# Kernel optimization log

Measured on AMD Instinct MI355X. Metric: run time of the kernel, lower is better.

## Reference

```python
import jax, jax.numpy as jnp
import numpy as np
import math

D_MODEL = 256
N_HEADS = 4
D_HEAD = D_MODEL // N_HEADS  # 64
TT_RANK = 4
BATCH = 4
SEQ = 2048


def _xavier(key, shape):
    fan_in, fan_out = shape[0], shape[-1]
    if len(shape) == 4:  # (H, d, d, r) treated roughly like dense xavier
        fan_in, fan_out = shape[1], shape[2] * shape[3]
    lim = math.sqrt(6.0 / (fan_in + fan_out))
    return jax.random.uniform(key, shape, jnp.float32, -lim, lim)


def setup_inputs() -> dict:
    key = jax.random.key(0)
    ks = jax.random.split(key, 12)
    inp = {
        "query": jax.random.normal(ks[0], (BATCH, SEQ, D_MODEL), jnp.float32),
        "key": jax.random.normal(ks[1], (BATCH, SEQ, D_MODEL), jnp.float32),
        "value": jax.random.normal(ks[2], (BATCH, SEQ, D_MODEL), jnp.float32),
        "Wq": _xavier(ks[3], (D_MODEL, D_MODEL)),
        "bq": jnp.zeros((D_MODEL,), jnp.float32),
        "Wk": _xavier(ks[4], (D_MODEL, D_MODEL)),
        "bk": jnp.zeros((D_MODEL,), jnp.float32),
        "Wv": _xavier(ks[5], (D_MODEL, D_MODEL)),
        "bv": jnp.zeros((D_MODEL,), jnp.float32),
        "W2": _xavier(ks[6], (N_HEADS, D_HEAD, D_HEAD, TT_RANK)),
        "alpha": jnp.float32(0.5),  # nonzero so interaction path is exercised
        "Wo": _xavier(ks[7], (D_MODEL, D_MODEL)),
        "bo": jnp.zeros((D_MODEL,), jnp.float32),
    }
    return inp


def reference(query, key, value, Wq, bq, Wk, bk, Wv, bv, W2, alpha, Wo, bo):
    B, Sq, _ = query.shape
    Sk = key.shape[1]
    H, Dh = N_HEADS, D_HEAD

    # projections -> (B, H, S, Dh)
    Q = (query @ Wq + bq).reshape(B, Sq, H, Dh).transpose(0, 2, 1, 3)
    K = (key @ Wk + bk).reshape(B, Sk, H, Dh).transpose(0, 2, 1, 3)
    V = (value @ Wv + bv).reshape(B, Sk, H, Dh).transpose(0, 2, 1, 3)

    scale = math.sqrt(Dh)
    scores = jnp.einsum('bhqd,bhkd->bhqk', Q, K) / scale  # (B,H,Sq,Sk)

    # rank-2 tensor interaction: Qp[b,h,q,a,r] = sum_d Q[b,h,q,d] W2[h,d,a,r]
    #                            Kp[b,h,k,a,r] = sum_e K[b,h,k,e] W2[h,a,e,r]
    Qp = jnp.einsum('bhqd,hdar->bhqar', Q, W2)
    Kp = jnp.einsum('bhke,haer->bhkar', K, W2)
    interaction = jnp.einsum('bhqar,bhkar->bhqk', Qp, Kp) / (Dh * scale)

    total_scores = scores + alpha * interaction
    attn = jax.nn.softmax(total_scores, axis=-1)

    out = jnp.einsum('bhqk,bhkd->bhqd', attn, V)
    out = out.transpose(0, 2, 1, 3).reshape(B, Sq, H * Dh)
    return out @ Wo + bo
```

## Files before the change

kernel.cpp:

```cpp
#include <hip/hip_runtime.h>
#include <hip/hip_bf16.h>

#define BB   4
#define SS   2048
#define DM   256
#define HH   4
#define DHH  64
#define KSPL 4
#define KLEN (SS / KSPL)

typedef unsigned short ushort_t;
typedef unsigned int   uint_t;
using short8   = __attribute__((ext_vector_type(8))) short;
using ushort8  = __attribute__((ext_vector_type(8))) unsigned short;
using ushort4v = __attribute__((ext_vector_type(4))) unsigned short;
using float4v  = __attribute__((ext_vector_type(4))) float;

__device__ __forceinline__ ushort_t f2bf(float f) {
  uint_t u = __float_as_uint(f);
  uint_t r = (u + 0x7FFFu + ((u >> 16) & 1u)) >> 16;
  return (ushort_t)r;
}

__global__ __launch_bounds__(256) void k_pre(
    const float* __restrict__ Wk, const float* __restrict__ Wv,
    const float* __restrict__ Wo, const float* __restrict__ Wq,
    const float* __restrict__ bq, const float* __restrict__ W2,
    const float* __restrict__ alpha_p,
    ushort_t* __restrict__ WkT, ushort_t* __restrict__ WvT,
    ushort_t* __restrict__ WoT, ushort_t* __restrict__ WcT,
    float* __restrict__ bc) {
  __shared__ float sT[64 * 65];
  __shared__ __align__(16) float sM[64];
  const int t = threadIdx.x;
  const int bi = blockIdx.x;
  if (bi < 48) {
    int m = bi >> 4, tile = bi & 15;
    int ot = tile >> 2, ct = tile & 3;
    const float* src = (m == 0) ? Wk : (m == 1) ? Wv : Wo;
    ushort_t* dst = (m == 0) ? WkT : (m == 1) ? WvT : WoT;
#pragma unroll
    for (int it = 0; it < 16; ++it) {
      int i = it * 4 + (t >> 6), j = t & 63;
      sT[i * 65 + j] = src[(ct * 64 + i) * 256 + ot * 64 + j];
    }
    __syncthreads();
#pragma unroll
    for (int it = 0; it < 16; ++it) {
      int jj = it * 4 + (t >> 6), ii = t & 63;
      dst[(ot * 64 + jj) * 256 + ct * 64 + ii] = f2bf(sT[ii * 65 + jj]);
    }
  } else {
    int o = bi - 48;
    int h = o >> 6, e = o & 63;
    if (t < 64) {
      const float* Wd = W2 + h * 16384 + t * 256;
      const float* We = W2 + h * 16384 + e * 4;
      float s = 0.f;
#pragma unroll 8
      for (int a = 0; a < 64; ++a) {
        float4 x = *(const float4*)(Wd + a * 4);
        float4 y = *(const float4*)(We + a * 256);
        s += x.x * y.x + x.y * y.y + x.z * y.z + x.w * y.w;
      }
      sM[t] = (t == e ? 0.125f : 0.f) + alpha_p[0] * (1.f / 512.f) * s;
    }
    __syncthreads();
    const float* Wrow = Wq + t * 256 + h * 64;
    float s = 0.f;
#pragma unroll
    for (int d4 = 0; d4 < 16; ++d4) {
      float4 x = *(const float4*)(Wrow + d4 * 4);
      float4 mm = *(const float4*)(sM + d4 * 4);
      s += x.x * mm.x + x.y * mm.y + x.z * mm.z + x.w * mm.w;
    }
    WcT[o * 256 + t] = f2bf(s);
    if (t == 0) {
      float sb = 0.f;
      for (int d = 0; d < 64; ++d) sb += bq[h * 64 + d] * sM[d];
      bc[o] = sb;
    }
  }
}

__global__ __launch_bounds__(256) void k_proj(
    const float* __restrict__ q_in, const float* __restrict__ k_in,
    const float* __restrict__ v_in,
    const ushort_t* __restrict__ WcT, const ushort_t* __restrict__ WkT,
    const ushort_t* __restrict__ WvT,
    const float* __restrict__ bc, const float* __restrict__ bk,
    const float* __restrict__ bv,
    ushort_t* __restrict__ Qa, ushort_t* __restrict__ Ka,
    ushort_t* __restrict__ VTg) {
  __shared__ ushort_t sX[64 * 256];
  const int t = threadIdx.x;
  const int w = t >> 6, lane = t & 63, g = lane >> 4, l16 = lane & 15;
  const int m = blockIdx.y;
  const int row0 = blockIdx.x * 64;
  const int b = row0 >> 11, s0 = row0 & (SS - 1);
  const float* src = (m == 0) ? q_in : (m == 1) ? k_in : v_in;
  const ushort_t* WT = (m == 0) ? WcT : (m == 1) ? WkT : WvT;
  const float* bias = (m == 0) ? bc : (m == 1) ? bk : bv;

#pragma unroll
  for (int it = 0; it < 8; ++it) {
    int blk = it * 256 + t;
    int r = blk >> 5, c16 = blk & 31;
    const float* p = src + (size_t)(row0 + r) * DM + c16 * 8;
    float4 a0 = *(const float4*)p, a1 = *(const float4*)(p + 4);
    ushort8 u;
    u[0] = f2bf(a0.x); u[1] = f2bf(a0.y); u[2] = f2bf(a0.z); u[3] = f2bf(a0.w);
    u[4] = f2bf(a1.x); u[5] = f2bf(a1.y); u[6] = f2bf(a1.z); u[7] = f2bf(a1.w);
    *(ushort8*)&sX[r * 256 + ((c16 ^ (r & 7)) << 3)] = u;
  }
  __syncthreads();

  short8 af[8];
  {
    int r = w * 16 + l16;
#pragma unroll
    for (int kc = 0; kc < 8; ++kc)
      af[kc] = *(const short8*)&sX[r * 256 + (((kc * 4 + g) ^ (r & 7)) << 3)];
  }

  float4v acc[16];
#pragma unroll
  for (int ct = 0; ct < 16; ++ct) acc[ct] = (float4v){0.f, 0.f, 0.f, 0.f};
#pragma unroll
  for (int ct = 0; ct < 16; ++ct) {
#pragma unroll
    for (int kc = 0; kc < 8; ++kc) {
      short8 bf = *(const short8*)&WT[(ct * 16 + l16) * 256 + kc * 32 + g * 8];
      acc[ct] = __builtin_amdgcn_mfma_f32_16x16x32_bf16(af[kc], bf, acc[ct],
                                                        0, 0, 0);
    }
  }
  __syncthreads();

#pragma unroll
  for (int ct = 0; ct < 16; ++ct) {
    int col = ct * 16 + l16;
    float bv = bias[col];
#pragma unroll
    for (int r4 = 0; r4 < 4; ++r4) {
      int row = w * 16 + g * 4 + r4;
      sX[row * 256 + (((col >> 3) ^ (row & 7)) << 3) + (col & 7)] =
          f2bf(acc[ct][r4] + bv);
    }
  }
  __syncthreads();

  if (m < 2) {
    ushort_t* dst = (m == 0) ? Qa : Ka;
#pragma unroll
    for (int it = 0; it < 8; ++it) {
      int blk = it * 256 + t;
      int r = blk >> 5, c16 = blk & 31;
      ushort8 u = *(const ushort8*)&sX[r * 256 + ((c16 ^ (r & 7)) << 3)];
      int h = c16 >> 3, dh = (c16 * 8) & 63;
      *(ushort8*)&dst[((size_t)(b * HH + h) * SS + s0 + r) * DHH + dh] = u;
    }
  } else {
#pragma unroll
    for (int it = 0; it < 8; ++it) {
      int idx = it * 256 + t;
      int col = idx >> 3, sblk = idx & 7;
      ushort8 u;
#pragma unroll
      for (int ji = 0; ji < 8; ++ji) {
        int row = sblk * 8 + ji;
        u[ji] = sX[row * 256 + (((col >> 3) ^ (row & 7)) << 3) + (col & 7)];
      }
      int h = col >> 6, dh = col & 63;
      *(ushort8*)&VTg[((size_t)(b * HH + h) * DHH + dh) * SS + s0 + sblk * 8] = u;
    }
  }
}

__global__ __launch_bounds__(256, 4) void k_attn(
    const ushort_t* __restrict__ Qa, const ushort_t* __restrict__ Ka,
    const ushort_t* __restrict__ VTg,
    float* __restrict__ Opart, float* __restrict__ lpart) {
  __shared__ ushort_t sKa[64 * 64];
  __shared__ ushort_t sVT[64 * 64];
  __shared__ ushort_t sPT[128 * 64];

  const int t = threadIdx.x;
  const int w = t >> 6, lane = t & 63, g = lane >> 4, l16 = lane & 15;
  const int bh = blockIdx.y;
  const int q0 = blockIdx.x * 128;
  const int ks = blockIdx.z;

  short8 qfrag[2][2];
#pragma unroll
  for (int s = 0; s < 2; ++s) {
    const ushort_t* qp =
        Qa + ((size_t)bh * SS + q0 + s * 64 + w * 16 + l16) * DHH + g * 8;
    qfrag[s][0] = *(const short8*)(qp);
    qfrag[s][1] = *(const short8*)(qp + 32);
  }

  const ushort_t* KaB = Ka + (size_t)bh * SS * DHH + (size_t)ks * KLEN * DHH;
  const ushort_t* VTB = VTg + (size_t)bh * DHH * SS + ks * KLEN;

  const int r0 = t >> 3, c0 = t & 7, r1 = r0 + 32;
  const int sw0 = r0 * 64 + ((c0 ^ (r0 & 7)) << 3);
  const int sw1 = r1 * 64 + ((c0 ^ (r1 & 7)) << 3);

  float l_run[2] = {0.f, 0.f};
  float4v oacc[2][4];
#pragma unroll
  for (int s = 0; s < 2; ++s)
#pragma unroll
    for (int dj = 0; dj < 4; ++dj) oacc[s][dj] = (float4v){0.f, 0.f, 0.f, 0.f};

  for (int kch = 0; kch < KLEN / 64; ++kch) {
    __syncthreads();
    {
      short8 k0 = *(const short8*)(KaB + (size_t)(kch * 64 + r0) * DHH + c0 * 8);
      short8 k1 = *(const short8*)(KaB + (size_t)(kch * 64 + r1) * DHH + c0 * 8);
      short8 v0 = *(const short8*)(VTB + (size_t)r0 * SS + kch * 64 + c0 * 8);
      short8 v1 = *(const short8*)(VTB + (size_t)r1 * SS + kch * 64 + c0 * 8);
      *(short8*)(sKa + sw0) = k0;
      *(short8*)(sKa + sw1) = k1;
      *(short8*)(sVT + sw0) = v0;
      *(short8*)(sVT + sw1) = v1;
    }
    __syncthreads();

    float4v sacc[2][4];
#pragma unroll
    for (int s = 0; s < 2; ++s)
#pragma unroll
      for (int kj = 0; kj < 4; ++kj)
        sacc[s][kj] = (float4v){-20.f, -20.f, -20.f, -20.f};
#pragma unroll
    for (int kc = 0; kc < 2; ++kc) {
#pragma unroll
      for (int kj = 0; kj < 4; ++kj) {
        int krow = kj * 16 + l16;
        short8 kf = *(const short8*)(sKa + krow * 64 +
                                     (((kc * 4 + g) ^ (krow & 7)) << 3));
        sacc[0][kj] = __builtin_amdgcn_mfma_f32_16x16x32_bf16(
            kf, qfrag[0][kc], sacc[0][kj], 0, 0, 0);
        sacc[1][kj] = __builtin_amdgcn_mfma_f32_16x16x32_bf16(
            kf, qfrag[1][kc], sacc[1][kj], 0, 0, 0);
      }
    }

#pragma unroll
    for (int s = 0; s < 2; ++s) {
      int qrow = s * 64 + w * 16 + l16;
      float lp = 0.f;
#pragma unroll
      for (int kj = 0; kj < 4; ++kj) {
        float p0 = __expf(sacc[s][kj][0]);
        float p1 = __expf(sacc[s][kj][1]);
        float p2 = __expf(sacc[s][kj][2]);
        float p3 = __expf(sacc[s][kj][3]);
        uint_t u01 = __builtin_amdgcn_perm(__float_as_uint(p1),
                                           __float_as_uint(p0), 0x07060302u);
        uint_t u23 = __builtin_amdgcn_perm(__float_as_uint(p3),
                                           __float_as_uint(p2), 0x07060302u);
        lp += __uint_as_float(__float_as_uint(p0) & 0xFFFF0000u);
        lp += __uint_as_float(__float_as_uint(p1) & 0xFFFF0000u);
        lp += __uint_as_float(__float_as_uint(p2) & 0xFFFF0000u);
        lp += __uint_as_float(__float_as_uint(p3) & 0xFFFF0000u);
        int kbase = kj * 16 + g * 4;
        uint2 pack; pack.x = u01; pack.y = u23;
        *(uint2*)(sPT + qrow * 64 + (((kbase >> 3) ^ (qrow & 7)) << 3) +
                  (kbase & 7)) = pack;
      }
      l_run[s] += lp;
    }

#pragma unroll
    for (int ck = 0; ck < 2; ++ck) {
      short8 vb[4];
#pragma unroll
      for (int dj = 0; dj < 4; ++dj) {
        int vrow = dj * 16 + l16;
        vb[dj] = *(const short8*)(sVT + vrow * 64 +
                                  (((ck * 4 + g) ^ (vrow & 7)) << 3));
      }
#pragma unroll
      for (int s = 0; s < 2; ++s) {
        int qrow = s * 64 + w * 16 + l16;
        short8 pa = *(const short8*)(sPT + qrow * 64 +
                                     (((ck * 4 + g) ^ (qrow & 7)) << 3));
#pragma unroll
        for (int dj = 0; dj < 4; ++dj)
          oacc[s][dj] = __builtin_amdgcn_mfma_f32_16x16x32_bf16(
              pa, vb[dj], oacc[s][dj], 0, 0, 0);
      }
    }
  }

  const int b = bh >> 2, h = bh & 3;
  float* Ob = Opart + (size_t)ks * (8192 * 256);
#pragma unroll
  for (int s = 0; s < 2; ++s) {
    l_run[s] += __shfl_xor(l_run[s], 16, 64);
    l_run[s] += __shfl_xor(l_run[s], 32, 64);
    if (g == 0)
      lpart[(size_t)ks * (8192 * 4) +
            ((size_t)b * SS + q0 + s * 64 + w * 16 + l16) * 4 + h] = l_run[s];
#pragma unroll
    for (int r = 0; r < 4; ++r) {
      size_t row = (size_t)b * SS + q0 + s * 64 + w * 16 + g * 4 + r;
#pragma unroll
      for (int dj = 0; dj < 4; ++dj)
        Ob[row * DM + h * DHH + dj * 16 + l16] = oacc[s][dj][r];
    }
  }
}

__global__ __launch_bounds__(512) void k_out(
    const float* __restrict__ Opart, const float* __restrict__ lpart,
    const ushort_t* __restrict__ WoT, const float* __restrict__ bo,
    float* __restrict__ Out) {
  __shared__ ushort_t sA[16 * 256];
  const int t = threadIdx.x;
  const int w = t >> 6, lane = t & 63, g = lane >> 4, l16 = lane & 15;
  const int row0 = blockIdx.x * 16;
  {
    int r = t >> 5, cf = (t & 31) * 8;
    size_t row = row0 + r;
    int h = cf >> 6;
    float l = 0.f;
    float s0 = 0.f, s1 = 0.f, s2 = 0.f, s3 = 0.f,
          s4 = 0.f, s5 = 0.f, s6 = 0.f, s7 = 0.f;
#pragma unroll
    for (int ks = 0; ks < KSPL; ++ks) {
      l += lpart[(size_t)ks * (8192 * 4) + row * 4 + h];
      const float* o = Opart + (size_t)ks * (8192 * 256) + row * DM + cf;
      float4 a0 = *(const float4*)o, a1 = *(const float4*)(o + 4);
      s0 += a0.x; s1 += a0.y; s2 += a0.z; s3 += a0.w;
      s4 += a1.x; s5 += a1.y; s6 += a1.z; s7 += a1.w;
    }
    float linv = 1.0f / l;
    ushort8 u;
    u[0] = f2bf(s0 * linv); u[1] = f2bf(s1 * linv);
    u[2] = f2bf(s2 * linv); u[3] = f2bf(s3 * linv);
    u[4] = f2bf(s4 * linv); u[5] = f2bf(s5 * linv);
    u[6] = f2bf(s6 * linv); u[7] = f2bf(s7 * linv);
    *(ushort8*)&sA[r * 256 + (((cf >> 3) ^ (r & 7)) << 3)] = u;
  }
  __syncthreads();

  float4v acc[2];
  acc[0] = (float4v){0.f, 0.f, 0.f, 0.f};
  acc[1] = (float4v){0.f, 0.f, 0.f, 0.f};
#pragma unroll
  for (int kc = 0; kc < 8; ++kc) {
    short8 af = *(const short8*)&sA[l16 * 256 + (((kc * 4 + g) ^ (l16 & 7)) << 3)];
#pragma unroll
    for (int ct = 0; ct < 2; ++ct) {
      int col = w * 32 + ct * 16 + l16;
      short8 bf = *(const short8*)&WoT[col * 256 + kc * 32 + g * 8];
      acc[ct] = __builtin_amdgcn_mfma_f32_16x16x32_bf16(af, bf, acc[ct], 0, 0, 0);
    }
  }
#pragma unroll
  for (int ct = 0; ct < 2; ++ct) {
    int col = w * 32 + ct * 16 + l16;
    float bv = bo[col];
#pragma unroll
    for (int r = 0; r < 4; ++r)
      Out[(size_t)(row0 + g * 4 + r) * DM + col] = acc[ct][r] + bv;
  }
}

extern "C" void kernel_launch(void* const* d_in, const int* in_sizes, int n_in,
                              void* d_out, int out_size, void* d_ws, size_t ws_size,
                              hipStream_t stream) {
  (void)in_sizes; (void)n_in; (void)out_size; (void)ws_size;
  const float* q_in  = (const float*)d_in[0];
  const float* k_in  = (const float*)d_in[1];
  const float* v_in  = (const float*)d_in[2];
  const float* Wq    = (const float*)d_in[3];
  const float* bq    = (const float*)d_in[4];
  const float* Wk    = (const float*)d_in[5];
  const float* bk    = (const float*)d_in[6];
  const float* Wv    = (const float*)d_in[7];
  const float* bv    = (const float*)d_in[8];
  const float* W2    = (const float*)d_in[9];
  const float* alpha = (const float*)d_in[10];
  const float* Wo    = (const float*)d_in[11];
  const float* bo    = (const float*)d_in[12];
  float* out = (float*)d_out;

  char* ws = (char*)d_ws;
  ushort_t* Qa    = (ushort_t*)ws;
  ushort_t* Ka    = (ushort_t*)(ws + 4194304);
  ushort_t* VTg   = (ushort_t*)(ws + 8388608);
  float*    Opart = (float*)(ws + 12582912);
  float*    lpart = (float*)(ws + 46137344);
  ushort_t* WkT   = (ushort_t*)(ws + 48234496);
  ushort_t* WvT   = (ushort_t*)(ws + 48365568);
  ushort_t* WoT   = (ushort_t*)(ws + 48496640);
  ushort_t* WcT   = (ushort_t*)(ws + 48627712);
  float*    bc    = (float*)(ws + 48758784);

  hipLaunchKernelGGL(k_pre, dim3(304), dim3(256), 0, stream,
                     Wk, Wv, Wo, Wq, bq, W2, alpha, WkT, WvT, WoT, WcT, bc);
  hipLaunchKernelGGL(k_proj, dim3(128, 3), dim3(256), 0, stream,
                     q_in, k_in, v_in, WcT, WkT, WvT, bc, bk, bv, Qa, Ka, VTg);
  hipLaunchKernelGGL(k_attn, dim3(SS / 128, BB * HH, KSPL), dim3(256), 0,
                     stream, Qa, Ka, VTg, Opart, lpart);
  hipLaunchKernelGGL(k_out, dim3(512), dim3(512), 0, stream,
                     Opart, lpart, WoT, bo, out);
}
```

Baseline: 173.7 us.

## Fuse all stages into one persistent kernel with grid-wide atomic barriers

```diff
diff --git a/kernel.cpp b/kernel.cpp
--- a/kernel.cpp
+++ b/kernel.cpp
@@ -6,14 +6,13 @@
 #define DM   256
 #define HH   4
 #define DHH  64
-#define KSPL 4
-#define KLEN (SS / KSPL)
+#define KSPL 2
+#define NBLK 512
 
 typedef unsigned short ushort_t;
 typedef unsigned int   uint_t;
 using short8   = __attribute__((ext_vector_type(8))) short;
 using ushort8  = __attribute__((ext_vector_type(8))) unsigned short;
-using ushort4v = __attribute__((ext_vector_type(4))) unsigned short;
 using float4v  = __attribute__((ext_vector_type(4))) float;
 
 __device__ __forceinline__ ushort_t f2bf(float f) {
@@ -22,352 +21,366 @@
   return (ushort_t)r;
 }
 
-__global__ __launch_bounds__(256) void k_pre(
-    const float* __restrict__ Wk, const float* __restrict__ Wv,
-    const float* __restrict__ Wo, const float* __restrict__ Wq,
-    const float* __restrict__ bq, const float* __restrict__ W2,
-    const float* __restrict__ alpha_p,
+__device__ __forceinline__ void gbar(uint_t* cnt, int idx) {
+  __syncthreads();
+  if (threadIdx.x == 0) {
+    __threadfence();
+    uint_t* p = cnt + idx * 32;
+    atomicAdd(p, 1u);
+    int guard = 0;
+    while (atomicAdd(p, 0u) < (uint_t)NBLK && guard < (1 << 22)) ++guard;
+    __threadfence();
+  }
+  __syncthreads();
+}
+
+__global__ __launch_bounds__(256, 2) void k_fused(
+    const float* __restrict__ q_in, const float* __restrict__ k_in,
+    const float* __restrict__ v_in,
+    const float* __restrict__ Wq, const float* __restrict__ bq,
+    const float* __restrict__ Wk, const float* __restrict__ bk,
+    const float* __restrict__ Wv, const float* __restrict__ bv,
+    const float* __restrict__ W2, const float* __restrict__ alpha_p,
+    const float* __restrict__ Wo, const float* __restrict__ bo,
+    ushort_t* __restrict__ Qa, ushort_t* __restrict__ Ka,
+    ushort_t* __restrict__ VTg,
+    float* __restrict__ Opart, float* __restrict__ lpart,
     ushort_t* __restrict__ WkT, ushort_t* __restrict__ WvT,
     ushort_t* __restrict__ WoT, ushort_t* __restrict__ WcT,
-    float* __restrict__ bc) {
-  __shared__ float sT[64 * 65];
-  __shared__ __align__(16) float sM[64];
+    float* __restrict__ bc, uint_t* __restrict__ bar,
+    float* __restrict__ Out) {
+  __shared__ __align__(16) ushort_t sBuf[64 * 256];
   const int t = threadIdx.x;
-  const int bi = blockIdx.x;
-  if (bi < 48) {
-    int m = bi >> 4, tile = bi & 15;
-    int ot = tile >> 2, ct = tile & 3;
-    const float* src = (m == 0) ? Wk : (m == 1) ? Wv : Wo;
-    ushort_t* dst = (m == 0) ? WkT : (m == 1) ? WvT : WoT;
-#pragma unroll
-    for (int it = 0; it < 16; ++it) {
-      int i = it * 4 + (t >> 6), j = t & 63;
-      sT[i * 65 + j] = src[(ct * 64 + i) * 256 + ot * 64 + j];
-    }
-    __syncthreads();
-#pragma unroll
-    for (int it = 0; it < 16; ++it) {
-      int jj = it * 4 + (t >> 6), ii = t & 63;
-      dst[(ot * 64 + jj) * 256 + ct * 64 + ii] = f2bf(sT[ii * 65 + jj]);
-    }
-  } else {
-    int o = bi - 48;
-    int h = o >> 6, e = o & 63;
-    if (t < 64) {
-      const float* Wd = W2 + h * 16384 + t * 256;
-      const float* We = W2 + h * 16384 + e * 4;
+  const int bid = blockIdx.x;
+  const int w = t >> 6, lane = t & 63, g = lane >> 4, l16 = lane & 15;
+
+  if (bid < 304) {
+    float* sT = (float*)sBuf;
+    float* sM = (float*)((char*)sBuf + 64 * 65 * 4);
+    if (bid < 48) {
+      int m = bid >> 4, tile = bid & 15;
+      int ot = tile >> 2, ct = tile & 3;
+      const float* src = (m == 0) ? Wk : (m == 1) ? Wv : Wo;
+      ushort_t* dst = (m == 0) ? WkT : (m == 1) ? WvT : WoT;
+#pragma unroll
+      for (int it = 0; it < 16; ++it) {
+        int i = it * 4 + (t >> 6), j = t & 63;
+        sT[i * 65 + j] = src[(ct * 64 + i) * 256 + ot * 64 + j];
+      }
+      __syncthreads();
+#pragma unroll
+      for (int it = 0; it < 16; ++it) {
+        int jj = it * 4 + (t >> 6), ii = t & 63;
+        dst[(ot * 64 + jj) * 256 + ct * 64 + ii] = f2bf(sT[ii * 65 + jj]);
+      }
+    } else {
+      int o = bid - 48;
+      int h = o >> 6, e = o & 63;
+      if (t < 64) {
+        const float* Wd = W2 + h * 16384 + t * 256;
+        const float* We = W2 + h * 16384 + e * 4;
+        float s = 0.f;
+#pragma unroll 8
+        for (int a = 0; a < 64; ++a) {
+          float4 x = *(const float4*)(Wd + a * 4);
+          float4 y = *(const float4*)(We + a * 256);
+          s += x.x * y.x + x.y * y.y + x.z * y.z + x.w * y.w;
+        }
+        sM[t] = (t == e ? 0.125f : 0.f) + alpha_p[0] * (1.f / 512.f) * s;
+      }
+      __syncthreads();
+      const float* Wrow = Wq + t * 256 + h * 64;
       float s = 0.f;
-#pragma unroll 8
-      for (int a = 0; a < 64; ++a) {
-        float4 x = *(const float4*)(Wd + a * 4);
-        float4 y = *(const float4*)(We + a * 256);
-        s += x.x * y.x + x.y * y.y + x.z * y.z + x.w * y.w;
-      }
-      sM[t] = (t == e ? 0.125f : 0.f) + alpha_p[0] * (1.f / 512.f) * s;
-    }
-    __syncthreads();
-    const float* Wrow = Wq + t * 256 + h * 64;
-    float s = 0.f;
-#pragma unroll
-    for (int d4 = 0; d4 < 16; ++d4) {
-      float4 x = *(const float4*)(Wrow + d4 * 4);
-      float4 mm = *(const float4*)(sM + d4 * 4);
-      s += x.x * mm.x + x.y * mm.y + x.z * mm.z + x.w * mm.w;
-    }
-    WcT[o * 256 + t] = f2bf(s);
-    if (t == 0) {
-      float sb = 0.f;
-      for (int d = 0; d < 64; ++d) sb += bq[h * 64 + d] * sM[d];
-      bc[o] = sb;
+#pragma unroll
+      for (int d4 = 0; d4 < 16; ++d4) {
+        float4 x = *(const float4*)(Wrow + d4 * 4);
+        float4 mm = *(const float4*)(sM + d4 * 4);
+        s += x.x * mm.x + x.y * mm.y + x.z * mm.z + x.w * mm.w;
+      }
+      WcT[o * 256 + t] = f2bf(s);
+      if (t == 0) {
+        float sb = 0.f;
+        for (int d = 0; d < 64; ++d) sb += bq[h * 64 + d] * sM[d];
+        bc[o] = sb;
+      }
     }
   }
-}
-
-__global__ __launch_bounds__(256) void k_proj(
-    const float* __restrict__ q_in, const float* __restrict__ k_in,
-    const float* __restrict__ v_in,
-    const ushort_t* __restrict__ WcT, const ushort_t* __restrict__ WkT,
-    const ushort_t* __restrict__ WvT,
-    const float* __restrict__ bc, const float* __restrict__ bk,
-    const float* __restrict__ bv,
-    ushort_t* __restrict__ Qa, ushort_t* __restrict__ Ka,
-    ushort_t* __restrict__ VTg) {
-  __shared__ ushort_t sX[64 * 256];
-  const int t = threadIdx.x;
-  const int w = t >> 6, lane = t & 63, g = lane >> 4, l16 = lane & 15;
-  const int m = blockIdx.y;
-  const int row0 = blockIdx.x * 64;
-  const int b = row0 >> 11, s0 = row0 & (SS - 1);
-  const float* src = (m == 0) ? q_in : (m == 1) ? k_in : v_in;
-  const ushort_t* WT = (m == 0) ? WcT : (m == 1) ? WkT : WvT;
-  const float* bias = (m == 0) ? bc : (m == 1) ? bk : bv;
-
-#pragma unroll
-  for (int it = 0; it < 8; ++it) {
-    int blk = it * 256 + t;
-    int r = blk >> 5, c16 = blk & 31;
-    const float* p = src + (size_t)(row0 + r) * DM + c16 * 8;
-    float4 a0 = *(const float4*)p, a1 = *(const float4*)(p + 4);
-    ushort8 u;
-    u[0] = f2bf(a0.x); u[1] = f2bf(a0.y); u[2] = f2bf(a0.z); u[3] = f2bf(a0.w);
-    u[4] = f2bf(a1.x); u[5] = f2bf(a1.y); u[6] = f2bf(a1.z); u[7] = f2bf(a1.w);
-    *(ushort8*)&sX[r * 256 + ((c16 ^ (r & 7)) << 3)] = u;
+  gbar(bar, 0);
+
+  {
+    const int row0 = bid * 16;
+    const int b = row0 >> 11, s0 = row0 & (SS - 1);
+    ushort_t* sX = sBuf;
+    for (int m = 0; m < 3; ++m) {
+      if (m) __syncthreads();
+      const float* src = (m == 0) ? q_in : (m == 1) ? k_in : v_in;
+      const ushort_t* WT = (m == 0) ? WcT : (m == 1) ? WkT : WvT;
+      const float* bias = (m == 0) ? bc : (m == 1) ? bk : bv;
+
+#pragma unroll
+      for (int it = 0; it < 2; ++it) {
+        int blk = it * 256 + t;
+        int r = blk >> 5, c16 = blk & 31;
+        const float* p = src + (size_t)(row0 + r) * DM + c16 * 8;
+        float4 a0 = *(const float4*)p, a1 = *(const float4*)(p + 4);
+        ushort8 u;
+        u[0] = f2bf(a0.x); u[1] = f2bf(a0.y); u[2] = f2bf(a0.z); u[3] = f2bf(a0.w);
+        u[4] = f2bf(a1.x); u[5] = f2bf(a1.y); u[6] = f2bf(a1.z); u[7] = f2bf(a1.w);
+        *(ushort8*)&sX[r * 256 + ((c16 ^ (r & 7)) << 3)] = u;
+      }
+      __syncthreads();
+
+      short8 af[8];
+#pragma unroll
+      for (int kc = 0; kc < 8; ++kc)
+        af[kc] = *(const short8*)&sX[l16 * 256 + (((kc * 4 + g) ^ (l16 & 7)) << 3)];
+
+      float4v acc[4];
+#pragma unroll
+      for (int ct = 0; ct < 4; ++ct) acc[ct] = (float4v){0.f, 0.f, 0.f, 0.f};
+#pragma unroll
+      for (int ct = 0; ct < 4; ++ct) {
+        int col = w * 64 + ct * 16 + l16;
+#pragma unroll
+        for (int kc = 0; kc < 8; ++kc) {
+          short8 bf = *(const short8*)&WT[col * 256 + kc * 32 + g * 8];
+          acc[ct] = __builtin_amdgcn_mfma_f32_16x16x32_bf16(af[kc], bf, acc[ct],
+                                                            0, 0, 0);
+        }
+      }
+      __syncthreads();
+
+#pragma unroll
+      for (int ct = 0; ct < 4; ++ct) {
+        int col = w * 64 + ct * 16 + l16;
+        float bvv = bias[col];
+#pragma unroll
+        for (int r4 = 0; r4 < 4; ++r4) {
+          int row = g * 4 + r4;
+          sX[row * 256 + (((col >> 3) ^ (row & 7)) << 3) + (col & 7)] =
+              f2bf(acc[ct][r4] + bvv);
+        }
+      }
+      __syncthreads();
+
+      if (m < 2) {
+        ushort_t* dst = (m == 0) ? Qa : Ka;
+#pragma unroll
+        for (int it = 0; it < 2; ++it) {
+          int blk = it * 256 + t;
+          int r = blk >> 5, c16 = blk & 31;
+          ushort8 u = *(const ushort8*)&sX[r * 256 + ((c16 ^ (r & 7)) << 3)];
+          int h = c16 >> 3, dh = (c16 & 7) * 8;
+          *(ushort8*)&dst[((size_t)(b * HH + h) * SS + s0 + r) * DHH + dh] = u;
+        }
+      } else {
+#pragma unroll
+        for (int it = 0; it < 2; ++it) {
+          int idx = it * 256 + t;
+          int col = idx >> 1, sblk = idx & 1;
+          ushort8 u;
+#pragma unroll
+          for (int ji = 0; ji < 8; ++ji) {
+            int row = sblk * 8 + ji;
+            u[ji] = sX[row * 256 + (((col >> 3) ^ (row & 7)) << 3) + (col & 7)];
+          }
+          int h = col >> 6, dh = col & 63;
+          *(ushort8*)&VTg[((size_t)(b * HH + h) * DHH + dh) * SS + s0 + sblk * 8] = u;
+        }
+      }
+    }
   }
-  __syncthreads();
-
-  short8 af[8];
+  gbar(bar, 1);
+
   {
-    int r = w * 16 + l16;
-#pragma unroll
-    for (int kc = 0; kc < 8; ++kc)
-      af[kc] = *(const short8*)&sX[r * 256 + (((kc * 4 + g) ^ (r & 7)) << 3)];
-  }
-
-  float4v acc[16];
-#pragma unroll
-  for (int ct = 0; ct < 16; ++ct) acc[ct] = (float4v){0.f, 0.f, 0.f, 0.f};
-#pragma unroll
-  for (int ct = 0; ct < 16; ++ct) {
-#pragma unroll
-    for (int kc = 0; kc < 8; ++kc) {
-      short8 bf = *(const short8*)&WT[(ct * 16 + l16) * 256 + kc * 32 + g * 8];
-      acc[ct] = __builtin_amdgcn_mfma_f32_16x16x32_bf16(af[kc], bf, acc[ct],
-                                                        0, 0, 0);
-    }
-  }
-  __syncthreads();
-
-#pragma unroll
-  for (int ct = 0; ct < 16; ++ct) {
-    int col = ct * 16 + l16;
-    float bv = bias[col];
-#pragma unroll
-    for (int r4 = 0; r4 < 4; ++r4) {
-      int row = w * 16 + g * 4 + r4;
-      sX[row * 256 + (((col >> 3) ^ (row & 7)) << 3) + (col & 7)] =
-          f2bf(acc[ct][r4] + bv);
-    }
-  }
-  __syncthreads();
-
-  if (m < 2) {
-    ushort_t* dst = (m == 0) ? Qa : Ka;
-#pragma unroll
-    for (int it = 0; it < 8; ++it) {
-      int blk = it * 256 + t;
-      int r = blk >> 5, c16 = blk & 31;
-      ushort8 u = *(const ushort8*)&sX[r * 256 + ((c16 ^ (r & 7)) << 3)];
-      int h = c16 >> 3, dh = (c16 * 8) & 63;
-      *(ushort8*)&dst[((size_t)(b * HH + h) * SS + s0 + r) * DHH + dh] = u;
-    }
-  } else {
-#pragma unroll
-    for (int it = 0; it < 8; ++it) {
-      int idx = it * 256 + t;
-      int col = idx >> 3, sblk = idx & 7;
-      ushort8 u;
-#pragma unroll
-      for (int ji = 0; ji < 8; ++ji) {
-        int row = sblk * 8 + ji;
-        u[ji] = sX[row * 256 + (((col >> 3) ^ (row & 7)) << 3) + (col & 7)];
-      }
-      int h = col >> 6, dh = col & 63;
-      *(ushort8*)&VTg[((size_t)(b * HH + h) * DHH + dh) * SS + s0 + sblk * 8] = u;
-    }
-  }
-}
-
-__global__ __launch_bounds__(256, 4) void k_attn(
-    const ushort_t* __restrict__ Qa, const ushort_t* __restrict__ Ka,
-    const ushort_t* __restrict__ VTg,
-    float* __restrict__ Opart, float* __restrict__ lpart) {
-  __shared__ ushort_t sKa[64 * 64];
-  __shared__ ushort_t sVT[64 * 64];
-  __shared__ ushort_t sPT[128 * 64];
-
-  const int t = threadIdx.x;
-  const int w = t >> 6, lane = t & 63, g = lane >> 4, l16 = lane & 15;
-  const int bh = blockIdx.y;
-  const int q0 = blockIdx.x * 128;
-  const int ks = blockIdx.z;
-
-  short8 qfrag[2][2];
-#pragma unroll
-  for (int s = 0; s < 2; ++s) {
-    const ushort_t* qp =
-        Qa + ((size_t)bh * SS + q0 + s * 64 + w * 16 + l16) * DHH + g * 8;
-    qfrag[s][0] = *(const short8*)(qp);
-    qfrag[s][1] = *(const short8*)(qp + 32);
-  }
-
-  const ushort_t* KaB = Ka + (size_t)bh * SS * DHH + (size_t)ks * KLEN * DHH;
-  const ushort_t* VTB = VTg + (size_t)bh * DHH * SS + ks * KLEN;
-
-  const int r0 = t >> 3, c0 = t & 7, r1 = r0 + 32;
-  const int sw0 = r0 * 64 + ((c0 ^ (r0 & 7)) << 3);
-  const int sw1 = r1 * 64 + ((c0 ^ (r1 & 7)) << 3);
-
-  float l_run[2] = {0.f, 0.f};
-  float4v oacc[2][4];
-#pragma unroll
-  for (int s = 0; s < 2; ++s)
-#pragma unroll
-    for (int dj = 0; dj < 4; ++dj) oacc[s][dj] = (float4v){0.f, 0.f, 0.f, 0.f};
-
-  for (int kch = 0; kch < KLEN / 64; ++kch) {
-    __syncthreads();
-    {
-      short8 k0 = *(const short8*)(KaB + (size_t)(kch * 64 + r0) * DHH + c0 * 8);
-      short8 k1 = *(const short8*)(KaB + (size_t)(kch * 64 + r1) * DHH + c0 * 8);
-      short8 v0 = *(const short8*)(VTB + (size_t)r0 * SS + kch * 64 + c0 * 8);
-      short8 v1 = *(const short8*)(VTB + (size_t)r1 * SS + kch * 64 + c0 * 8);
-      *(short8*)(sKa + sw0) = k0;
-      *(short8*)(sKa + sw1) = k1;
-      *(short8*)(sVT + sw0) = v0;
-      *(short8*)(sVT + sw1) = v1;
-    }
-    __syncthreads();
-
-    float4v sacc[2][4];
+    int ks = bid >> 8;
+    int rem = bid & 255;
+    int qt = rem & 15, bh = rem >> 4;
+    int q0 = qt * 128;
+    int kstart = ks * 1024;
+    ushort_t* sKa = sBuf;
+    ushort_t* sVT = sBuf + 4096;
+    ushort_t* sPT = sBuf + 8192;
+
+    short8 qfrag[2][2];
+#pragma unroll
+    for (int s = 0; s < 2; ++s) {
+      const ushort_t* qp =
+          Qa + ((size_t)bh * SS + q0 + s * 64 + w * 16 + l16) * DHH + g * 8;
+      qfrag[s][0] = *(const short8*)(qp);
+      qfrag[s][1] = *(const short8*)(qp + 32);
+    }
+    const ushort_t* KaB = Ka + (size_t)bh * SS * DHH + (size_t)kstart * DHH;
+    const ushort_t* VTB = VTg + (size_t)bh * DHH * SS + kstart;
+
+    const int r0 = t >> 3, c0 = t & 7, r1 = r0 + 32;
+    const int sw0 = r0 * 64 + ((c0 ^ (r0 & 7)) << 3);
+    const int sw1 = r1 * 64 + ((c0 ^ (r1 & 7)) << 3);
+
+    float l_run[2] = {0.f, 0.f};
+    float4v oacc[2][4];
 #pragma unroll
     for (int s = 0; s < 2; ++s)
 #pragma unroll
-      for (int kj = 0; kj < 4; ++kj)
-        sacc[s][kj] = (float4v){-20.f, -20.f, -20.f, -20.f};
-#pragma unroll
-    for (int kc = 0; kc < 2; ++kc) {
-#pragma unroll
-      for (int kj = 0; kj < 4; ++kj) {
-        int krow = kj * 16 + l16;
-        short8 kf = *(const short8*)(sKa + krow * 64 +
-                                     (((kc * 4 + g) ^ (krow & 7)) << 3));
-        sacc[0][kj] = __builtin_amdgcn_mfma_f32_16x16x32_bf16(
-            kf, qfrag[0][kc], sacc[0][kj], 0, 0, 0);
-        sacc[1][kj] = __builtin_amdgcn_mfma_f32_16x16x32_bf16(
-            kf, qfrag[1][kc], sacc[1][kj], 0, 0, 0);
-      }
-    }
-
-#pragma unroll
-    for (int s = 0; s < 2; ++s) {
-      int qrow = s * 64 + w * 16 + l16;
-      float lp = 0.f;
-#pragma unroll
-      for (int kj = 0; kj < 4; ++kj) {
-        float p0 = __expf(sacc[s][kj][0]);
-        float p1 = __expf(sacc[s][kj][1]);
-        float p2 = __expf(sacc[s][kj][2]);
-        float p3 = __expf(sacc[s][kj][3]);
-        uint_t u01 = __builtin_amdgcn_perm(__float_as_uint(p1),
-                                           __float_as_uint(p0), 0x07060302u);
-        uint_t u23 = __builtin_amdgcn_perm(__float_as_uint(p3),
-                                           __float_as_uint(p2), 0x07060302u);
-        lp += __uint_as_float(__float_as_uint(p0) & 0xFFFF0000u);
-        lp += __uint_as_float(__float_as_uint(p1) & 0xFFFF0000u);
-        lp += __uint_as_float(__float_as_uint(p2) & 0xFFFF0000u);
-        lp += __uint_as_float(__float_as_uint(p3) & 0xFFFF0000u);
-        int kbase = kj * 16 + g * 4;
-        uint2 pack; pack.x = u01; pack.y = u23;
-        *(uint2*)(sPT + qrow * 64 + (((kbase >> 3) ^ (qrow & 7)) << 3) +
-                  (kbase & 7)) = pack;
-      }
-      l_run[s] += lp;
-    }
-
-#pragma unroll
-    for (int ck = 0; ck < 2; ++ck) {
-      short8 vb[4];
-#pragma unroll
-      for (int dj = 0; dj < 4; ++dj) {
-        int vrow = dj * 16 + l16;
-        vb[dj] = *(const short8*)(sVT + vrow * 64 +
-                                  (((ck * 4 + g) ^ (vrow & 7)) << 3));
-      }
+      for (int dj = 0; dj < 4; ++dj) oacc[s][dj] = (float4v){0.f, 0.f, 0.f, 0.f};
+
+    for (int kch = 0; kch < 16; ++kch) {
+      __syncthreads();
+      {
+        short8 k0 = *(const short8*)(KaB + (size_t)(kch * 64 + r0) * DHH + c0 * 8);
+        short8 k1 = *(const short8*)(KaB + (size_t)(kch * 64 + r1) * DHH + c0 * 8);
+        short8 v0 = *(const short8*)(VTB + (size_t)r0 * SS + kch * 64 + c0 * 8);
+        short8 v1 = *(const short8*)(VTB + (size_t)r1 * SS + kch * 64 + c0 * 8);
+        *(short8*)(sKa + sw0) = k0;
+        *(short8*)(sKa + sw1) = k1;
+        *(short8*)(sVT + sw0) = v0;
+        *(short8*)(sVT + sw1) = v1;
+      }
+      __syncthreads();
+
+      float4v sacc[2][4];
+#pragma unroll
+      for (int s = 0; s < 2; ++s)
+#pragma unroll
+        for (int kj = 0; kj < 4; ++kj)
+          sacc[s][kj] = (float4v){-20.f, -20.f, -20.f, -20.f};
+#pragma unroll
+      for (int kc = 0; kc < 2; ++kc) {
+#pragma unroll
+        for (int kj = 0; kj < 4; ++kj) {
+          int krow = kj * 16 + l16;
+          short8 kf = *(const short8*)(sKa + krow * 64 +
+                                       (((kc * 4 + g) ^ (krow & 7)) << 3));
+          sacc[0][kj] = __builtin_amdgcn_mfma_f32_16x16x32_bf16(
+              kf, qfrag[0][kc], sacc[0][kj], 0, 0, 0);
+          sacc[1][kj] = __builtin_amdgcn_mfma_f32_16x16x32_bf16(
+              kf, qfrag[1][kc], sacc[1][kj], 0, 0, 0);
+        }
+      }
+
 #pragma unroll
       for (int s = 0; s < 2; ++s) {
         int qrow = s * 64 + w * 16 + l16;
-        short8 pa = *(const short8*)(sPT + qrow * 64 +
-                                     (((ck * 4 + g) ^ (qrow & 7)) << 3));
+        float lp = 0.f;
+#pragma unroll
+        for (int kj = 0; kj < 4; ++kj) {
+          float p0 = __expf(sacc[s][kj][0]);
+          float p1 = __expf(sacc[s][kj][1]);
+          float p2 = __expf(sacc[s][kj][2]);
+          float p3 = __expf(sacc[s][kj][3]);
+          uint_t u01 = __builtin_amdgcn_perm(__float_as_uint(p1),
+                                             __float_as_uint(p0), 0x07060302u);
+          uint_t u23 = __builtin_amdgcn_perm(__float_as_uint(p3),
+                                             __float_as_uint(p2), 0x07060302u);
+          lp += __uint_as_float(__float_as_uint(p0) & 0xFFFF0000u);
+          lp += __uint_as_float(__float_as_uint(p1) & 0xFFFF0000u);
+          lp += __uint_as_float(__float_as_uint(p2) & 0xFFFF0000u);
+          lp += __uint_as_float(__float_as_uint(p3) & 0xFFFF0000u);
+          int kbase = kj * 16 + g * 4;
+          uint2 pack; pack.x = u01; pack.y = u23;
+          *(uint2*)(sPT + qrow * 64 + (((kbase >> 3) ^ (qrow & 7)) << 3) +
+                    (kbase & 7)) = pack;
+        }
+        l_run[s] += lp;
+      }
+
+#pragma unroll
+      for (int ck = 0; ck < 2; ++ck) {
+        short8 vb[4];
+#pragma unroll
+        for (int dj = 0; dj < 4; ++dj) {
+          int vrow = dj * 16 + l16;
+          vb[dj] = *(const short8*)(sVT + vrow * 64 +
+                                    (((ck * 4 + g) ^ (vrow & 7)) << 3));
+        }
+#pragma unroll
+        for (int s = 0; s < 2; ++s) {
+          int qrow = s * 64 + w * 16 + l16;
+          short8 pa = *(const short8*)(sPT + qrow * 64 +
+                                       (((ck * 4 + g) ^ (qrow & 7)) << 3));
+#pragma unroll
+          for (int dj = 0; dj < 4; ++dj)
+            oacc[s][dj] = __builtin_amdgcn_mfma_f32_16x16x32_bf16(
+                pa, vb[dj], oacc[s][dj], 0, 0, 0);
+        }
+      }
+    }
+
+    const int b = bh >> 2, h = bh & 3;
+    float* Ob = Opart + (size_t)ks * (8192 * 256);
+#pragma unroll
+    for (int s = 0; s < 2; ++s) {
+      l_run[s] += __shfl_xor(l_run[s], 16, 64);
+      l_run[s] += __shfl_xor(l_run[s], 32, 64);
+      if (g == 0)
+        lpart[(size_t)ks * (8192 * 4) +
+              ((size_t)b * SS + q0 + s * 64 + w * 16 + l16) * 4 + h] = l_run[s];
+#pragma unroll
+      for (int r = 0; r < 4; ++r) {
+        size_t row = (size_t)b * SS + q0 + s * 64 + w * 16 + g * 4 + r;
 #pragma unroll
         for (int dj = 0; dj < 4; ++dj)
-          oacc[s][dj] = __builtin_amdgcn_mfma_f32_16x16x32_bf16(
-              pa, vb[dj], oacc[s][dj], 0, 0, 0);
+          Ob[row * DM + h * DHH + dj * 16 + l16] = oacc[s][dj][r];
       }
     }
   }
-
-  const int b = bh >> 2, h = bh & 3;
-  float* Ob = Opart + (size_t)ks * (8192 * 256);
-#pragma unroll
-  for (int s = 0; s < 2; ++s) {
-    l_run[s] += __shfl_xor(l_run[s], 16, 64);
-    l_run[s] += __shfl_xor(l_run[s], 32, 64);
-    if (g == 0)
-      lpart[(size_t)ks * (8192 * 4) +
-            ((size_t)b * SS + q0 + s * 64 + w * 16 + l16) * 4 + h] = l_run[s];
-#pragma unroll
-    for (int r = 0; r < 4; ++r) {
-      size_t row = (size_t)b * SS + q0 + s * 64 + w * 16 + g * 4 + r;
-#pragma unroll
-      for (int dj = 0; dj < 4; ++dj)
-        Ob[row * DM + h * DHH + dj * 16 + l16] = oacc[s][dj][r];
-    }
-  }
-}
-
-__global__ __launch_bounds__(512) void k_out(
-    const float* __restrict__ Opart, const float* __restrict__ lpart,
-    const ushort_t* __restrict__ WoT, const float* __restrict__ bo,
-    float* __restrict__ Out) {
-  __shared__ ushort_t sA[16 * 256];
-  const int t = threadIdx.x;
-  const int w = t >> 6, lane = t & 63, g = lane >> 4, l16 = lane & 15;
-  const int row0 = blockIdx.x * 16;
+  gbar(bar, 2);
+
   {
-    int r = t >> 5, cf = (t & 31) * 8;
-    size_t row = row0 + r;
-    int h = cf >> 6;
-    float l = 0.f;
-    float s0 = 0.f, s1 = 0.f, s2 = 0.f, s3 = 0.f,
-          s4 = 0.f, s5 = 0.f, s6 = 0.f, s7 = 0.f;
-#pragma unroll
-    for (int ks = 0; ks < KSPL; ++ks) {
-      l += lpart[(size_t)ks * (8192 * 4) + row * 4 + h];
-      const float* o = Opart + (size_t)ks * (8192 * 256) + row * DM + cf;
-      float4 a0 = *(const float4*)o, a1 = *(const float4*)(o + 4);
-      s0 += a0.x; s1 += a0.y; s2 += a0.z; s3 += a0.w;
-      s4 += a1.x; s5 += a1.y; s6 += a1.z; s7 += a1.w;
-    }
-    float linv = 1.0f / l;
-    ushort8 u;
-    u[0] = f2bf(s0 * linv); u[1] = f2bf(s1 * linv);
-    u[2] = f2bf(s2 * linv); u[3] = f2bf(s3 * linv);
-    u[4] = f2bf(s4 * linv); u[5] = f2bf(s5 * linv);
-    u[6] = f2bf(s6 * linv); u[7] = f2bf(s7 * linv);
-    *(ushort8*)&sA[r * 256 + (((cf >> 3) ^ (r & 7)) << 3)] = u;
-  }
-  __syncthreads();
-
-  float4v acc[2];
-  acc[0] = (float4v){0.f, 0.f, 0.f, 0.f};
-  acc[1] = (float4v){0.f, 0.f, 0.f, 0.f};
-#pragma unroll
-  for (int kc = 0; kc < 8; ++kc) {
-    short8 af = *(const short8*)&sA[l16 * 256 + (((kc * 4 + g) ^ (l16 & 7)) << 3)];
-#pragma unroll
-    for (int ct = 0; ct < 2; ++ct) {
-      int col = w * 32 + ct * 16 + l16;
-      short8 bf = *(const short8*)&WoT[col * 256 + kc * 32 + g * 8];
-      acc[ct] = __builtin_amdgcn_mfma_f32_16x16x32_bf16(af, bf, acc[ct], 0, 0, 0);
-    }
-  }
-#pragma unroll
-  for (int ct = 0; ct < 2; ++ct) {
-    int col = w * 32 + ct * 16 + l16;
-    float bv = bo[col];
-#pragma unroll
-    for (int r = 0; r < 4; ++r)
-      Out[(size_t)(row0 + g * 4 + r) * DM + col] = acc[ct][r] + bv;
+    ushort_t* sA = sBuf;
+    const int row0 = bid * 16;
+#pragma unroll
+    for (int it = 0; it < 2; ++it) {
+      int idx = it * 256 + t;
+      int r = idx >> 5, cf = (idx & 31) * 8;
+      size_t row = row0 + r;
+      int h = cf >> 6;
+      float l = 0.f;
+      float s0 = 0.f, s1 = 0.f, s2 = 0.f, s3 = 0.f,
+            s4 = 0.f, s5 = 0.f, s6 = 0.f, s7 = 0.f;
+#pragma unroll
+      for (int ks = 0; ks < KSPL; ++ks) {
+        l += lpart[(size_t)ks * (8192 * 4) + row * 4 + h];
+        const float* o = Opart + (size_t)ks * (8192 * 256) + row * DM + cf;
+        float4 a0 = *(const float4*)o, a1 = *(const float4*)(o + 4);
+        s0 += a0.x; s1 += a0.y; s2 += a0.z; s3 += a0.w;
+        s4 += a1.x; s5 += a1.y; s6 += a1.z; s7 += a1.w;
+      }
+      float linv = 1.0f / l;
+      ushort8 u;
+      u[0] = f2bf(s0 * linv); u[1] = f2bf(s1 * linv);
+      u[2] = f2bf(s2 * linv); u[3] = f2bf(s3 * linv);
+      u[4] = f2bf(s4 * linv); u[5] = f2bf(s5 * linv);
+      u[6] = f2bf(s6 * linv); u[7] = f2bf(s7 * linv);
+      *(ushort8*)&sA[r * 256 + (((cf >> 3) ^ (r & 7)) << 3)] = u;
+    }
+    __syncthreads();
+
+    short8 af[8];
+#pragma unroll
+    for (int kc = 0; kc < 8; ++kc)
+      af[kc] = *(const short8*)&sA[l16 * 256 + (((kc * 4 + g) ^ (l16 & 7)) << 3)];
+    float4v acc[4];
+#pragma unroll
+    for (int ct = 0; ct < 4; ++ct) acc[ct] = (float4v){0.f, 0.f, 0.f, 0.f};
+#pragma unroll
+    for (int ct = 0; ct < 4; ++ct) {
+      int col = w * 64 + ct * 16 + l16;
+#pragma unroll
+      for (int kc = 0; kc < 8; ++kc) {
+        short8 bf = *(const short8*)&WoT[col * 256 + kc * 32 + g * 8];
+        acc[ct] = __builtin_amdgcn_mfma_f32_16x16x32_bf16(af[kc], bf, acc[ct],
+                                                          0, 0, 0);
+      }
+    }
+#pragma unroll
+    for (int ct = 0; ct < 4; ++ct) {
+      int col = w * 64 + ct * 16 + l16;
+      float bvv = bo[col];
+#pragma unroll
+      for (int r = 0; r < 4; ++r)
+        Out[(size_t)(row0 + g * 4 + r) * DM + col] = acc[ct][r] + bvv;
+    }
   }
 }
 
@@ -395,19 +408,18 @@
   ushort_t* Ka    = (ushort_t*)(ws + 4194304);
   ushort_t* VTg   = (ushort_t*)(ws + 8388608);
   float*    Opart = (float*)(ws + 12582912);
-  float*    lpart = (float*)(ws + 46137344);
-  ushort_t* WkT   = (ushort_t*)(ws + 48234496);
-  ushort_t* WvT   = (ushort_t*)(ws + 48365568);
-  ushort_t* WoT   = (ushort_t*)(ws + 48496640);
-  ushort_t* WcT   = (ushort_t*)(ws + 48627712);
-  float*    bc    = (float*)(ws + 48758784);
-
-  hipLaunchKernelGGL(k_pre, dim3(304), dim3(256), 0, stream,
-                     Wk, Wv, Wo, Wq, bq, W2, alpha, WkT, WvT, WoT, WcT, bc);
-  hipLaunchKernelGGL(k_proj, dim3(128, 3), dim3(256), 0, stream,
-                     q_in, k_in, v_in, WcT, WkT, WvT, bc, bk, bv, Qa, Ka, VTg);
-  hipLaunchKernelGGL(k_attn, dim3(SS / 128, BB * HH, KSPL), dim3(256), 0,
-                     stream, Qa, Ka, VTg, Opart, lpart);
-  hipLaunchKernelGGL(k_out, dim3(512), dim3(512), 0, stream,
-                     Opart, lpart, WoT, bo, out);
+  float*    lpart = (float*)(ws + 29360128);
+  ushort_t* WkT   = (ushort_t*)(ws + 29622272);
+  ushort_t* WvT   = (ushort_t*)(ws + 29753344);
+  ushort_t* WoT   = (ushort_t*)(ws + 29884416);
+  ushort_t* WcT   = (ushort_t*)(ws + 30015488);
+  float*    bc    = (float*)(ws + 30146560);
+  uint_t*   bar   = (uint_t*)(ws + 30147584);
+
+  hipMemsetAsync(bar, 0, 512, stream);
+
+  hipLaunchKernelGGL(k_fused, dim3(NBLK), dim3(256), 0, stream,
+                     q_in, k_in, v_in, Wq, bq, Wk, bk, Wv, bv, W2, alpha,
+                     Wo, bo, Qa, Ka, VTg, Opart, lpart,
+                     WkT, WvT, WoT, WcT, bc, bar, out);
 }
```

Result: slower. 307.2 us (+76.9%).
